# Kernel optimization log

Measured on AMD Instinct MI355X. Metric: run time of the kernel, lower is better.

## Reference

```python
import jax, jax.numpy as jnp
import numpy as np

B, ENC_LEN, DEC_LEN = 4, 1024, 256
ENC_H, DEC_H, ATTN = 1024, 1024, 256


def setup_inputs() -> dict:
    key = jax.random.key(0)
    k1, k2, k3, k4, k5, k6 = jax.random.split(key, 6)
    scale = 0.02
    return {
        "encoded_seq": jax.random.normal(k1, (B, ENC_LEN, ENC_H), jnp.float32),
        "decoder_state": jax.random.normal(k2, (B, DEC_LEN, DEC_H), jnp.float32),
        "input_pad_mask": jnp.ones((B, ENC_LEN), jnp.float32),
        "Wh": jax.random.normal(k3, (ENC_H, ATTN), jnp.float32) * scale,
        "Ws": jax.random.normal(k4, (DEC_H, ATTN), jnp.float32) * scale,
        "bs": jax.random.normal(k5, (ATTN,), jnp.float32) * scale,
        "v": jax.random.normal(k6, (ATTN,), jnp.float32) * scale,
    }


def reference(encoded_seq, decoder_state, input_pad_mask, Wh, Ws, bs, v):
    # projections: [B, dec, A] and [B, enc, A]
    proj_dec = jnp.einsum('bdh,ha->bda', decoder_state, Ws) + bs
    proj_enc = jnp.einsum('beh,ha->bea', encoded_seq, Wh)
    # additive score: tanh(broadcast add) then dot with selector vector v
    added = jnp.tanh(proj_dec[:, :, None, :] + proj_enc[:, None, :, :])  # [B,dec,enc,A]
    attn_logits = jnp.einsum('bdea,a->bde', added, v)                    # [B,dec,enc]
    attn_weights = jax.nn.softmax(attn_logits, axis=-1)
    attn_weights2 = attn_weights * input_pad_mask[:, None, :]
    attn_renorm = attn_weights2 / jnp.sum(attn_weights2, axis=-1, keepdims=True)
    context = jnp.einsum('bde,beh->bdh', attn_renorm, encoded_seq)       # [B,dec,enc_h]
    return context, attn_renorm
```

## Files before the change

### kernel.cpp

```cpp
#include <hip/hip_runtime.h>
#include <hip/hip_bf16.h>

#define BB 4
#define ENC_LEN 1024
#define DEC_LEN 256
#define ENC_H 1024
#define ATTN_A 256

#define C2F 2.8853900817779268f

typedef short bf16x8 __attribute__((ext_vector_type(8)));
typedef float f32x4 __attribute__((ext_vector_type(4)));
typedef unsigned int u32x2 __attribute__((ext_vector_type(2)));

union Q2D {
  uint4 q;
  u32x2 d[2];
};
union BF8 {
  u32x2 d[2];
  bf16x8 v;
};

static __device__ __forceinline__ unsigned short f2bf(float x) {
  union {
    float f;
    unsigned int u;
  } c;
  c.f = x;
  unsigned int r = c.u + 0x7FFFu + ((c.u >> 16) & 1u);
  return (unsigned short)(r >> 16);
}

__global__ __launch_bounds__(256) void prep_k(
    const float* __restrict__ Wh, const float* __restrict__ Ws,
    const float* __restrict__ enc, const float* __restrict__ dec,
    unsigned short* __restrict__ WhT, unsigned short* __restrict__ WsT,
    unsigned short* __restrict__ encT, unsigned short* __restrict__ encB,
    unsigned short* __restrict__ decB) {
  __shared__ unsigned short T[64][68];
  const int wb = blockIdx.x;
  const int t = threadIdx.x;
  const int lr = t >> 4;
  const int lc4 = (t & 15) * 4;

  if (wb >= 1152) {
    const int q = wb - 1152;
    const int r0 = (q >> 4) * 64;
    const int c0 = (q & 15) * 64;
#pragma unroll
    for (int p = 0; p < 4; ++p) {
      const int r = lr + p * 16;
      const float4 v = *(const float4*)&dec[(long)(r0 + r) * ENC_H + c0 + lc4];
      ushort4 o;
      o.x = f2bf(v.x);
      o.y = f2bf(v.y);
      o.z = f2bf(v.z);
      o.w = f2bf(v.w);
      *(ushort4*)&decB[(long)(r0 + r) * ENC_H + c0 + lc4] = o;
    }
    return;
  }

  const float* in;
  unsigned short* out;
  unsigned short* out2 = nullptr;
  int R, C, bx, by;
  if (wb < 128) {
    in = (wb < 64) ? Wh : Ws;
    out = (wb < 64) ? WhT : WsT;
    const int tt = wb & 63;
    R = ENC_H;
    C = ATTN_A;
    bx = tt & 3;
    by = tt >> 2;
  } else {
    const int tt0 = wb - 128;
    const int b = tt0 >> 8;
    const int tt = tt0 & 255;
    in = enc + (long)b * ENC_LEN * ENC_H;
    out = encT + (long)b * ENC_H * ENC_LEN;
    out2 = encB + (long)b * ENC_LEN * ENC_H;
    R = ENC_LEN;
    C = ENC_H;
    bx = tt & 15;
    by = tt >> 4;
  }
  const int r0 = by * 64;
  const int c0 = bx * 64;

#pragma unroll
  for (int p = 0; p < 4; ++p) {
    const int r = lr + p * 16;
    const float4 v = *(const float4*)&in[(long)(r0 + r) * C + c0 + lc4];
    ushort4 o;
    o.x = f2bf(v.x);
    o.y = f2bf(v.y);
    o.z = f2bf(v.z);
    o.w = f2bf(v.w);
    *(ushort4*)&T[r][lc4] = o;
    if (out2) *(ushort4*)&out2[(long)(r0 + r) * C + c0 + lc4] = o;
  }
  __syncthreads();
#pragma unroll
  for (int p = 0; p < 4; ++p) {
    const int c = lr + p * 16;
    ushort4 o;
    o.x = T[lc4 + 0][c];
    o.y = T[lc4 + 1][c];
    o.z = T[lc4 + 2][c];
    o.w = T[lc4 + 3][c];
    *(ushort4*)&out[(long)(c0 + c) * R + r0 + lc4] = o;
  }
}

__global__ __launch_bounds__(256) void pgemm(const unsigned short* __restrict__ decB,
                                             const unsigned short* __restrict__ encB,
                                             const unsigned short* __restrict__ WsT,
                                             const unsigned short* __restrict__ WhT,
                                             float* __restrict__ pdP,
                                             float* __restrict__ peP) {
  __shared__ unsigned short As[64][36];
  __shared__ unsigned short Bs[64][36];
  __shared__ float Cs[64][68];

  const int s = blockIdx.z;
  const bool isPD = blockIdx.y < 16;
  const unsigned short* A = isPD ? decB : encB;
  const unsigned short* BT = isPD ? WsT : WhT;
  const int m0 = (isPD ? blockIdx.y : (blockIdx.y - 16)) * 64;
  const int n0 = blockIdx.x * 64;
  const int kb = s * 512;

  const int tid = threadIdx.x;
  const int lane = tid & 63;
  const int wave = tid >> 6;
  const int quad = lane >> 4;
  const int l16 = lane & 15;
  const int wm = (wave >> 1) * 32;
  const int wn = (wave & 1) * 32;
  const int sr = tid >> 2;
  const int sk = (tid & 3) * 8;

  f32x4 acc[2][2] = {{{0.f, 0.f, 0.f, 0.f}, {0.f, 0.f, 0.f, 0.f}},
                     {{0.f, 0.f, 0.f, 0.f}, {0.f, 0.f, 0.f, 0.f}}};

  const unsigned short* Ap = A + (long)(m0 + sr) * ENC_H + kb + sk;
  const unsigned short* Bp = BT + (long)(n0 + sr) * ENC_H + kb + sk;

  Q2D av, bv;
  av.q = *(const uint4*)(Ap);
  bv.q = *(const uint4*)(Bp);

  for (int k0 = 0; k0 < 512; k0 += 32) {
    __syncthreads();
    *(u32x2*)&As[sr][sk] = av.d[0];
    *(u32x2*)&As[sr][sk + 4] = av.d[1];
    *(u32x2*)&Bs[sr][sk] = bv.d[0];
    *(u32x2*)&Bs[sr][sk + 4] = bv.d[1];
    const int kn = (k0 + 32 < 512) ? (k0 + 32) : 0;
    av.q = *(const uint4*)(Ap + kn);
    bv.q = *(const uint4*)(Bp + kn);
    __syncthreads();

    bf16x8 af[2], bfr[2];
#pragma unroll
    for (int i = 0; i < 2; ++i) {
      BF8 t;
      t.d[0] = *(const u32x2*)&As[wm + i * 16 + l16][quad * 8];
      t.d[1] = *(const u32x2*)&As[wm + i * 16 + l16][quad * 8 + 4];
      af[i] = t.v;
    }
#pragma unroll
    for (int j = 0; j < 2; ++j) {
      BF8 t;
      t.d[0] = *(const u32x2*)&Bs[wn + j * 16 + l16][quad * 8];
      t.d[1] = *(const u32x2*)&Bs[wn + j * 16 + l16][quad * 8 + 4];
      bfr[j] = t.v;
    }
#pragma unroll
    for (int i = 0; i < 2; ++i)
#pragma unroll
      for (int j = 0; j < 2; ++j)
        acc[i][j] = __builtin_amdgcn_mfma_f32_16x16x32_bf16(af[i], bfr[j], acc[i][j],
                                                            0, 0, 0);
  }

  if (isPD) {
    float* out = pdP + (long)s * (1024 * ATTN_A);
#pragma unroll
    for (int j = 0; j < 2; ++j) {
      const int col = n0 + wn + j * 16 + l16;
#pragma unroll
      for (int i = 0; i < 2; ++i) {
        const int row = m0 + wm + i * 16 + quad * 4;
#pragma unroll
        for (int r = 0; r < 4; ++r)
          out[(long)(row + r) * ATTN_A + col] = C2F * acc[i][j][r];
      }
    }
  } else {
    __syncthreads();
#pragma unroll
    for (int i = 0; i < 2; ++i)
#pragma unroll
      for (int j = 0; j < 2; ++j)
#pragma unroll
        for (int r = 0; r < 4; ++r)
          Cs[wn + j * 16 + l16][wm + i * 16 + quad * 4 + r] = C2F * acc[i][j][r];
    __syncthreads();
    const int gb = m0 >> 10;
    const int e0 = m0 & 1023;
    const int et = e0 >> 8;
    const int eoff = e0 & 255;
    float* out = peP + (long)s * (BB * ATTN_A * ENC_LEN) +
                 (long)gb * (ATTN_A * ENC_LEN) + (long)et * (ATTN_A * 256);
#pragma unroll
    for (int p = 0; p < 4; ++p) {
      const int arow = (tid >> 4) + p * 16;
      const int e4 = (tid & 15) * 4;
      const float4 o = *(const float4*)&Cs[arow][e4];
      *(float4*)&out[(long)(n0 + arow) * 256 + eoff + e4] = o;
    }
  }
}

__global__ __launch_bounds__(256) void logits_k(const float* __restrict__ peP,
                                                const float* __restrict__ pdP,
                                                const float* __restrict__ v,
                                                const float* __restrict__ bs,
                                                float* __restrict__ p0,
                                                float* __restrict__ p1,
                                                float* __restrict__ p2,
                                                float* __restrict__ p3) {
  const int tid = threadIdx.x;
  const int et = blockIdx.x;
  const int e = et * 256 + tid;
  const int d0 = blockIdx.y * 8;
  const int b = blockIdx.z >> 2;
  const int aq = blockIdx.z & 3;
  const int a0 = aq * 64;

  __shared__ float EdT[8][64];
  __shared__ float vv[64];

  {
    const int a = tid & 63;
    const int dh = tid >> 6;
    const float cb = C2F * bs[a0 + a];
#pragma unroll
    for (int j = 0; j < 2; ++j) {
      const int dd = dh * 2 + j;
      const long idx = (long)(b * DEC_LEN + d0 + dd) * ATTN_A + a0 + a;
      EdT[dd][a] =
          __builtin_amdgcn_exp2f(pdP[idx] + pdP[idx + 1024 * ATTN_A] + cb);
    }
    if (dh == 0) vv[a] = -2.0f * v[a0 + a];
  }
  __syncthreads();

  float acc[8] = {0.f, 0.f, 0.f, 0.f, 0.f, 0.f, 0.f, 0.f};
  const float* pe0 = peP + (long)b * (ATTN_A * ENC_LEN) + (long)et * (ATTN_A * 256) +
                     (long)a0 * 256 + tid;
  const float* pe1 = pe0 + (long)BB * ATTN_A * ENC_LEN;

  float pA0[4], pA1[4], pB0[4], pB1[4];
#pragma unroll
  for (int u = 0; u < 4; ++u) {
    pA0[u] = pe0[u * 256];
    pA1[u] = pe1[u * 256];
    pB0[u] = pe0[(4 + u) * 256];
    pB1[u] = pe1[(4 + u) * 256];
  }

  for (int a4 = 0; a4 < 64; a4 += 4) {
    float Ee[4];
#pragma unroll
    for (int u = 0; u < 4; ++u) Ee[u] = __builtin_amdgcn_exp2f(pA0[u] + pA1[u]);
    const int an = (a4 + 8 < 64) ? (a4 + 8) : 0;
#pragma unroll
    for (int u = 0; u < 4; ++u) {
      pA0[u] = pB0[u];
      pA1[u] = pB1[u];
      pB0[u] = pe0[(an + u) * 256];
      pB1[u] = pe1[(an + u) * 256];
    }
    const float4 v4 = *(const float4*)&vv[a4];

#pragma unroll
    for (int dd = 0; dd < 8; ++dd) {
      const float4 ed = *(const float4*)&EdT[dd][a4];
      const float dn0 = fmaf(ed.x, Ee[0], 1.0f);
      const float dn1 = fmaf(ed.y, Ee[1], 1.0f);
      const float dn2 = fmaf(ed.z, Ee[2], 1.0f);
      const float dn3 = fmaf(ed.w, Ee[3], 1.0f);
      const float x12 = dn0 * dn1;
      const float x34 = dn2 * dn3;
      float t1 = v4.x * dn1;
      t1 = fmaf(v4.y, dn0, t1);
      float t2 = v4.z * dn3;
      t2 = fmaf(v4.w, dn2, t2);
      float num = t1 * x34;
      num = fmaf(t2, x12, num);
      const float D = x12 * x34;
      const float r = __builtin_amdgcn_rcpf(D);
      acc[dd] = fmaf(num, r, acc[dd]);
    }
  }

  float* po = (aq == 0) ? p0 : (aq == 1) ? p1 : (aq == 2) ? p2 : p3;
  const long base = ((long)(b * DEC_LEN + d0) * ENC_LEN) + e;
#pragma unroll
  for (int dd = 0; dd < 8; ++dd) po[base + (long)dd * ENC_LEN] = acc[dd];
}

__global__ __launch_bounds__(256) void softmax4_k(float* __restrict__ p0,
                                                  const float* __restrict__ p1,
                                                  const float* __restrict__ p2,
                                                  const float* __restrict__ p3,
                                                  const float* __restrict__ mask,
                                                  unsigned short* __restrict__ attnB) {
  const int row = blockIdx.x;
  const int b = row >> 8;
  const int tid = threadIdx.x;
  float* rp = p0 + (long)row * ENC_LEN;
  const float* rq1 = p1 + (long)row * ENC_LEN;
  const float* rq2 = p2 + (long)row * ENC_LEN;
  const float* rq3 = p3 + (long)row * ENC_LEN;
  const float* mp = mask + b * ENC_LEN;
  unsigned short* rb = attnB + (long)row * ENC_LEN;

  float l[4], m[4];
#pragma unroll
  for (int j = 0; j < 4; ++j) {
    const int i = tid + 256 * j;
    l[j] = (rp[i] + rq1[i]) + (rq2[i] + rq3[i]);
    m[j] = mp[i];
  }

  __shared__ float redmax[4];
  __shared__ float redsum[4];
  const int lane = tid & 63;
  const int wid = tid >> 6;

  float tm = fmaxf(fmaxf(l[0], l[1]), fmaxf(l[2], l[3]));
#pragma unroll
  for (int off = 1; off < 64; off <<= 1) tm = fmaxf(tm, __shfl_xor(tm, off, 64));
  if (lane == 0) redmax[wid] = tm;
  __syncthreads();
  const float rmax = fmaxf(fmaxf(redmax[0], redmax[1]), fmaxf(redmax[2], redmax[3]));

  const float LOG2E = 1.4426950408889634f;
  float p[4];
  float ts = 0.f;
#pragma unroll
  for (int j = 0; j < 4; ++j) {
    p[j] = __builtin_amdgcn_exp2f((l[j] - rmax) * LOG2E) * m[j];
    ts += p[j];
  }
#pragma unroll
  for (int off = 1; off < 64; off <<= 1) ts += __shfl_xor(ts, off, 64);
  if (lane == 0) redsum[wid] = ts;
  __syncthreads();
  const float rsum = redsum[0] + redsum[1] + redsum[2] + redsum[3];

  const float inv = 1.0f / rsum;
#pragma unroll
  for (int j = 0; j < 4; ++j) {
    const float w = p[j] * inv;
    rp[tid + 256 * j] = w;
    rb[tid + 256 * j] = f2bf(w);
  }
}

__global__ __launch_bounds__(256) void cgemm(const unsigned short* __restrict__ attnB,
                                             const unsigned short* __restrict__ encT,
                                             float* __restrict__ cP) {
  __shared__ unsigned short As[64][36];
  __shared__ unsigned short Bs[64][36];

  const int b = blockIdx.z >> 1;
  const int s = blockIdx.z & 1;
  const int kb = s * 512;
  const unsigned short* A = attnB + (long)b * DEC_LEN * ENC_LEN;
  const unsigned short* BT = encT + (long)b * ENC_H * ENC_LEN;
  float* C = cP + (long)s * (BB * DEC_LEN * ENC_H) + (long)b * DEC_LEN * ENC_H;

  const int tid = threadIdx.x;
  const int lane = tid & 63;
  const int wave = tid >> 6;
  const int quad = lane >> 4;
  const int l16 = lane & 15;
  const int wm = (wave >> 1) * 32;
  const int wn = (wave & 1) * 32;
  const int m0 = blockIdx.y * 64;
  const int n0 = blockIdx.x * 64;
  const int sr = tid >> 2;
  const int sk = (tid & 3) * 8;

  f32x4 acc[2][2] = {{{0.f, 0.f, 0.f, 0.f}, {0.f, 0.f, 0.f, 0.f}},
                     {{0.f, 0.f, 0.f, 0.f}, {0.f, 0.f, 0.f, 0.f}}};

  const unsigned short* Ap = A + (long)(m0 + sr) * ENC_LEN + kb + sk;
  const unsigned short* Bp = BT + (long)(n0 + sr) * ENC_LEN + kb + sk;

  Q2D av, bv;
  av.q = *(const uint4*)(Ap);
  bv.q = *(const uint4*)(Bp);

  for (int k0 = 0; k0 < 512; k0 += 32) {
    __syncthreads();
    *(u32x2*)&As[sr][sk] = av.d[0];
    *(u32x2*)&As[sr][sk + 4] = av.d[1];
    *(u32x2*)&Bs[sr][sk] = bv.d[0];
    *(u32x2*)&Bs[sr][sk + 4] = bv.d[1];
    const int kn = (k0 + 32 < 512) ? (k0 + 32) : 0;
    av.q = *(const uint4*)(Ap + kn);
    bv.q = *(const uint4*)(Bp + kn);
    __syncthreads();

    bf16x8 af[2], bfr[2];
#pragma unroll
    for (int i = 0; i < 2; ++i) {
      BF8 t;
      t.d[0] = *(const u32x2*)&As[wm + i * 16 + l16][quad * 8];
      t.d[1] = *(const u32x2*)&As[wm + i * 16 + l16][quad * 8 + 4];
      af[i] = t.v;
    }
#pragma unroll
    for (int j = 0; j < 2; ++j) {
      BF8 t;
      t.d[0] = *(const u32x2*)&Bs[wn + j * 16 + l16][quad * 8];
      t.d[1] = *(const u32x2*)&Bs[wn + j * 16 + l16][quad * 8 + 4];
      bfr[j] = t.v;
    }
#pragma unroll
    for (int i = 0; i < 2; ++i)
#pragma unroll
      for (int j = 0; j < 2; ++j)
        acc[i][j] = __builtin_amdgcn_mfma_f32_16x16x32_bf16(af[i], bfr[j], acc[i][j],
                                                            0, 0, 0);
  }

#pragma unroll
  for (int j = 0; j < 2; ++j) {
    const int col = n0 + wn + j * 16 + l16;
#pragma unroll
    for (int i = 0; i < 2; ++i) {
      const int row = m0 + wm + i * 16 + quad * 4;
#pragma unroll
      for (int r = 0; r < 4; ++r) C[(long)(row + r) * ENC_H + col] = acc[i][j][r];
    }
  }
}

__global__ __launch_bounds__(256) void creduce(const float* __restrict__ cP,
                                               float* __restrict__ ctx) {
  const long i = ((long)blockIdx.x * 256 + threadIdx.x) * 4;
  const float4 x = *(const float4*)&cP[i];
  const float4 y = *(const float4*)&cP[i + (long)BB * DEC_LEN * ENC_H];
  float4 o;
  o.x = x.x + y.x;
  o.y = x.y + y.y;
  o.z = x.z + y.z;
  o.w = x.w + y.w;
  *(float4*)&ctx[i] = o;
}

template <int OMODE, bool BIAS>
__global__ __launch_bounds__(256) void gemm64(const float* __restrict__ A,
                                              const float* __restrict__ B,
                                              const float* __restrict__ bias,
                                              float* __restrict__ C,
                                              int K, int lda, int ldb, int ldc,
                                              long sA, long sB, long sC) {
  const int bz = blockIdx.z;
  A += (long)bz * sA;
  B += (long)bz * sB;
  C += (long)bz * sC;

  const int tid = threadIdx.x;
  const int tx = tid & 15;
  const int ty = tid >> 4;

  __shared__ float As2[16][64];
  __shared__ float Bs2[16][64];

  float acc[4][4];
#pragma unroll
  for (int i = 0; i < 4; ++i)
#pragma unroll
    for (int j = 0; j < 4; ++j) acc[i][j] = 0.f;

  const int ar = tid >> 2;
  const int ak4 = (tid & 3) << 2;
  const int br = tid >> 4;
  const int bn4 = (tid & 15) << 2;

  const float* Aload = A + (long)(blockIdx.y * 64 + ar) * lda + ak4;
  const float* Bload = B + (long)br * ldb + blockIdx.x * 64 + bn4;

  for (int k0 = 0; k0 < K; k0 += 16) {
    const float4 av = *(const float4*)(Aload + k0);
    const float4 bv = *(const float4*)(Bload + (long)k0 * ldb);
    __syncthreads();
    As2[ak4 + 0][ar] = av.x;
    As2[ak4 + 1][ar] = av.y;
    As2[ak4 + 2][ar] = av.z;
    As2[ak4 + 3][ar] = av.w;
    *(float4*)&Bs2[br][bn4] = bv;
    __syncthreads();
#pragma unroll
    for (int kk = 0; kk < 16; ++kk) {
      const float4 a4 = *(const float4*)&As2[kk][ty << 2];
      const float4 b4 = *(const float4*)&Bs2[kk][tx << 2];
      const float am[4] = {a4.x, a4.y, a4.z, a4.w};
      const float bn[4] = {b4.x, b4.y, b4.z, b4.w};
#pragma unroll
      for (int i = 0; i < 4; ++i)
#pragma unroll
        for (int j = 0; j < 4; ++j) acc[i][j] = fmaf(am[i], bn[j], acc[i][j]);
    }
  }

  if (OMODE == 0) {
    const int row0 = blockIdx.y * 64 + (ty << 2);
    const int col0 = blockIdx.x * 64 + (tx << 2);
    float4 bb4 = make_float4(0.f, 0.f, 0.f, 0.f);
    if (BIAS) bb4 = *(const float4*)&bias[col0];
#pragma unroll
    for (int i = 0; i < 4; ++i) {
      float4 o;
      o.x = acc[i][0] + bb4.x;
      o.y = acc[i][1] + bb4.y;
      o.z = acc[i][2] + bb4.z;
      o.w = acc[i][3] + bb4.w;
      *(float4*)&C[(long)(row0 + i) * ldc + col0] = o;
    }
  } else {
#pragma unroll
    for (int i = 0; i < 4; ++i) {
      const int gr = blockIdx.y * 64 + (ty << 2) + i;
      const int b = gr >> 10;
      const int e = gr & 1023;
#pragma unroll
      for (int j = 0; j < 4; ++j) {
        const int col = blockIdx.x * 64 + (tx << 2) + j;
        C[(long)b * (ATTN_A * ENC_LEN) + (long)col * ENC_LEN + e] = acc[i][j];
      }
    }
  }
}

__global__ __launch_bounds__(256) void logits_fb(const float* __restrict__ peT,
                                                 const float* __restrict__ pd,
                                                 const float* __restrict__ v,
                                                 float* __restrict__ out) {
  const int tid = threadIdx.x;
  const int e = blockIdx.x * 256 + tid;
  const int d0 = blockIdx.y * 8;
  const int b = blockIdx.z;

  __shared__ float cpd[ATTN_A][8];
  __shared__ float vv[ATTN_A];

  {
    const int a = tid;
#pragma unroll
    for (int dd = 0; dd < 8; ++dd)
      cpd[a][dd] = C2F * pd[((b * DEC_LEN + d0 + dd) * ATTN_A) + a];
    vv[a] = -2.0f * v[a];
  }
  __syncthreads();

  float acc[8] = {0.f, 0.f, 0.f, 0.f, 0.f, 0.f, 0.f, 0.f};
  const float* pe = peT + (long)b * (ATTN_A * ENC_LEN) + e;

  for (int a = 0; a < ATTN_A; a += 4) {
    float pes[4];
#pragma unroll
    for (int u = 0; u < 4; ++u) pes[u] = pe[(long)(a + u) * ENC_LEN];
#pragma unroll
    for (int u = 0; u < 4; ++u) {
      const float cpe = C2F * pes[u];
      const float vu = vv[a + u];
      const float4 c0 = *(const float4*)&cpd[a + u][0];
      const float4 c1 = *(const float4*)&cpd[a + u][4];
      const float cd[8] = {c0.x, c0.y, c0.z, c0.w, c1.x, c1.y, c1.z, c1.w};
#pragma unroll
      for (int dd = 0; dd < 8; ++dd) {
        const float x = cd[dd] + cpe;
        const float ex = __builtin_amdgcn_exp2f(x);
        const float r = __builtin_amdgcn_rcpf(ex + 1.0f);
        acc[dd] = fmaf(vu, r, acc[dd]);
      }
    }
  }

  const long base = ((long)(b * DEC_LEN + d0) * ENC_LEN) + e;
#pragma unroll
  for (int dd = 0; dd < 8; ++dd) out[base + (long)dd * ENC_LEN] = acc[dd];
}

__global__ __launch_bounds__(256) void softmax_fb(float* __restrict__ attn,
                                                  const float* __restrict__ mask) {
  const int row = blockIdx.x;
  const int b = row >> 8;
  const int tid = threadIdx.x;
  float* rp = attn + (long)row * ENC_LEN;
  const float* mp = mask + b * ENC_LEN;

  float l[4], m[4];
#pragma unroll
  for (int j = 0; j < 4; ++j) {
    l[j] = rp[tid + 256 * j];
    m[j] = mp[tid + 256 * j];
  }

  __shared__ float redmax[4];
  __shared__ float redsum[4];
  const int lane = tid & 63;
  const int wid = tid >> 6;

  float tm = fmaxf(fmaxf(l[0], l[1]), fmaxf(l[2], l[3]));
#pragma unroll
  for (int off = 1; off < 64; off <<= 1) tm = fmaxf(tm, __shfl_xor(tm, off, 64));
  if (lane == 0) redmax[wid] = tm;
  __syncthreads();
  const float rmax = fmaxf(fmaxf(redmax[0], redmax[1]), fmaxf(redmax[2], redmax[3]));

  const float LOG2E = 1.4426950408889634f;
  float p[4];
  float ts = 0.f;
#pragma unroll
  for (int j = 0; j < 4; ++j) {
    p[j] = __builtin_amdgcn_exp2f((l[j] - rmax) * LOG2E) * m[j];
    ts += p[j];
  }
#pragma unroll
  for (int off = 1; off < 64; off <<= 1) ts += __shfl_xor(ts, off, 64);
  if (lane == 0) redsum[wid] = ts;
  __syncthreads();
  const float rsum = redsum[0] + redsum[1] + redsum[2] + redsum[3];

  const float inv = 1.0f / rsum;
#pragma unroll
  for (int j = 0; j < 4; ++j) rp[tid + 256 * j] = p[j] * inv;
}

extern "C" void kernel_launch(void* const* d_in, const int* in_sizes, int n_in,
                              void* d_out, int out_size, void* d_ws, size_t ws_size,
                              hipStream_t stream) {
  const float* enc = (const float*)d_in[0];
  const float* dec = (const float*)d_in[1];
  const float* mask = (const float*)d_in[2];
  const float* Wh = (const float*)d_in[3];
  const float* Ws = (const float*)d_in[4];
  const float* bs = (const float*)d_in[5];
  const float* v = (const float*)d_in[6];

  float* ctx = (float*)d_out;
  float* attn = ctx + (long)BB * DEC_LEN * ENC_H;

  const long N_PD = 2L * 1024 * ATTN_A;
  const long N_PE = 2L * BB * ATTN_A * ENC_LEN;
  const long N_P1 = (long)BB * DEC_LEN * ENC_LEN;
  const long N_CP = 2L * BB * DEC_LEN * ENC_H;
  const long N_ENC = (long)BB * ENC_H * ENC_LEN;
  const long N_W = (long)ATTN_A * ENC_H;
  const long N_DEC = 1024L * ENC_H;
  const long N_ATT = (long)BB * DEC_LEN * ENC_LEN;
  const size_t FAST_WS = (N_PD + N_PE + 3 * N_P1 + N_CP) * 4 +
                         (N_ENC + 2 * N_W + N_ENC + N_DEC + N_ATT) * 2;

  if (ws_size >= FAST_WS) {
    float* pdP = (float*)d_ws;
    float* peP = pdP + N_PD;
    float* p1 = peP + N_PE;
    float* p2 = p1 + N_P1;
    float* p3 = p2 + N_P1;
    float* cP = p3 + N_P1;
    unsigned short* encT = (unsigned short*)(cP + N_CP);
    unsigned short* WhT = encT + N_ENC;
    unsigned short* WsT = WhT + N_W;
    unsigned short* encB = WsT + N_W;
    unsigned short* decB = encB + N_ENC;
    unsigned short* attnB = decB + N_DEC;

    prep_k<<<dim3(1408, 1, 1), 256, 0, stream>>>(Wh, Ws, enc, dec, WhT, WsT, encT,
                                                 encB, decB);
    pgemm<<<dim3(4, 80, 2), 256, 0, stream>>>(decB, encB, WsT, WhT, pdP, peP);
    logits_k<<<dim3(4, 32, BB * 4), 256, 0, stream>>>(peP, pdP, v, bs, attn, p1, p2,
                                                      p3);
    softmax4_k<<<dim3(BB * DEC_LEN, 1, 1), 256, 0, stream>>>(attn, p1, p2, p3, mask,
                                                             attnB);
    cgemm<<<dim3(16, 4, BB * 2), 256, 0, stream>>>(attnB, encT, cP);
    creduce<<<dim3(1024, 1, 1), 256, 0, stream>>>(cP, ctx);
  } else {
    float* pd = (float*)d_ws;
    float* peT = pd + (long)BB * DEC_LEN * ATTN_A;

    gemm64<0, true><<<dim3(ATTN_A / 64, (BB * DEC_LEN) / 64, 1), 256, 0, stream>>>(
        dec, Ws, bs, pd, ENC_H, ENC_H, ATTN_A, ATTN_A, 0, 0, 0);
    gemm64<1, false><<<dim3(ATTN_A / 64, (BB * ENC_LEN) / 64, 1), 256, 0, stream>>>(
        enc, Wh, nullptr, peT, ENC_H, ENC_H, ATTN_A, 0, 0, 0, 0);
    logits_fb<<<dim3(ENC_LEN / 256, DEC_LEN / 8, BB), 256, 0, stream>>>(peT, pd, v,
                                                                        attn);
    softmax_fb<<<dim3(BB * DEC_LEN, 1, 1), 256, 0, stream>>>(attn, mask);
    gemm64<0, false><<<dim3(ENC_H / 64, DEC_LEN / 64, BB), 256, 0, stream>>>(
        attn, enc, nullptr, ctx, ENC_LEN, ENC_LEN, ENC_H, ENC_H,
        (long)DEC_LEN * ENC_LEN, (long)ENC_LEN * ENC_H, (long)DEC_LEN * ENC_H);
  }
}
```

Measured before the change: 144.3 us.

## Replace split-K with smaller M tiles in projection and context GEMMs

```diff
diff --git a/kernel.cpp b/kernel.cpp
--- a/kernel.cpp
+++ b/kernel.cpp
@@ -120,56 +120,55 @@
                                              const unsigned short* __restrict__ WhT,
                                              float* __restrict__ pdP,
                                              float* __restrict__ peP) {
-  __shared__ unsigned short As[64][36];
+  __shared__ unsigned short As[32][36];
   __shared__ unsigned short Bs[64][36];
-  __shared__ float Cs[64][68];
-
-  const int s = blockIdx.z;
-  const bool isPD = blockIdx.y < 16;
+  __shared__ float Cs[64][36];
+
+  const bool isPD = blockIdx.y < 32;
   const unsigned short* A = isPD ? decB : encB;
   const unsigned short* BT = isPD ? WsT : WhT;
-  const int m0 = (isPD ? blockIdx.y : (blockIdx.y - 16)) * 64;
+  const int m0 = (isPD ? blockIdx.y : (blockIdx.y - 32)) * 32;
   const int n0 = blockIdx.x * 64;
-  const int kb = s * 512;
 
   const int tid = threadIdx.x;
   const int lane = tid & 63;
   const int wave = tid >> 6;
   const int quad = lane >> 4;
   const int l16 = lane & 15;
-  const int wm = (wave >> 1) * 32;
+  const int wm = (wave >> 1) * 16;
   const int wn = (wave & 1) * 32;
   const int sr = tid >> 2;
+  const int ar = (tid >> 2) & 31;
   const int sk = (tid & 3) * 8;
 
-  f32x4 acc[2][2] = {{{0.f, 0.f, 0.f, 0.f}, {0.f, 0.f, 0.f, 0.f}},
-                     {{0.f, 0.f, 0.f, 0.f}, {0.f, 0.f, 0.f, 0.f}}};
-
-  const unsigned short* Ap = A + (long)(m0 + sr) * ENC_H + kb + sk;
-  const unsigned short* Bp = BT + (long)(n0 + sr) * ENC_H + kb + sk;
+  f32x4 acc[2] = {{0.f, 0.f, 0.f, 0.f}, {0.f, 0.f, 0.f, 0.f}};
+
+  const unsigned short* Ap = A + (long)(m0 + ar) * ENC_H + sk;
+  const unsigned short* Bp = BT + (long)(n0 + sr) * ENC_H + sk;
 
   Q2D av, bv;
-  av.q = *(const uint4*)(Ap);
+  if (tid < 128) av.q = *(const uint4*)(Ap);
   bv.q = *(const uint4*)(Bp);
 
-  for (int k0 = 0; k0 < 512; k0 += 32) {
+  for (int k0 = 0; k0 < 1024; k0 += 32) {
     __syncthreads();
-    *(u32x2*)&As[sr][sk] = av.d[0];
-    *(u32x2*)&As[sr][sk + 4] = av.d[1];
+    if (tid < 128) {
+      *(u32x2*)&As[ar][sk] = av.d[0];
+      *(u32x2*)&As[ar][sk + 4] = av.d[1];
+    }
     *(u32x2*)&Bs[sr][sk] = bv.d[0];
     *(u32x2*)&Bs[sr][sk + 4] = bv.d[1];
-    const int kn = (k0 + 32 < 512) ? (k0 + 32) : 0;
-    av.q = *(const uint4*)(Ap + kn);
+    const int kn = (k0 + 32 < 1024) ? (k0 + 32) : 0;
+    if (tid < 128) av.q = *(const uint4*)(Ap + kn);
     bv.q = *(const uint4*)(Bp + kn);
     __syncthreads();
 
-    bf16x8 af[2], bfr[2];
-#pragma unroll
-    for (int i = 0; i < 2; ++i) {
+    bf16x8 af, bfr[2];
+    {
       BF8 t;
-      t.d[0] = *(const u32x2*)&As[wm + i * 16 + l16][quad * 8];
-      t.d[1] = *(const u32x2*)&As[wm + i * 16 + l16][quad * 8 + 4];
-      af[i] = t.v;
+      t.d[0] = *(const u32x2*)&As[wm + l16][quad * 8];
+      t.d[1] = *(const u32x2*)&As[wm + l16][quad * 8 + 4];
+      af = t.v;
     }
 #pragma unroll
     for (int j = 0; j < 2; ++j) {
@@ -179,46 +178,36 @@
       bfr[j] = t.v;
     }
 #pragma unroll
-    for (int i = 0; i < 2; ++i)
-#pragma unroll
-      for (int j = 0; j < 2; ++j)
-        acc[i][j] = __builtin_amdgcn_mfma_f32_16x16x32_bf16(af[i], bfr[j], acc[i][j],
-                                                            0, 0, 0);
+    for (int j = 0; j < 2; ++j)
+      acc[j] = __builtin_amdgcn_mfma_f32_16x16x32_bf16(af, bfr[j], acc[j], 0, 0, 0);
   }
 
   if (isPD) {
-    float* out = pdP + (long)s * (1024 * ATTN_A);
 #pragma unroll
     for (int j = 0; j < 2; ++j) {
       const int col = n0 + wn + j * 16 + l16;
-#pragma unroll
-      for (int i = 0; i < 2; ++i) {
-        const int row = m0 + wm + i * 16 + quad * 4;
-#pragma unroll
-        for (int r = 0; r < 4; ++r)
-          out[(long)(row + r) * ATTN_A + col] = C2F * acc[i][j][r];
-      }
+      const int row = m0 + wm + quad * 4;
+#pragma unroll
+      for (int r = 0; r < 4; ++r)
+        pdP[(long)(row + r) * ATTN_A + col] = C2F * acc[j][r];
     }
   } else {
-    __syncthreads();
-#pragma unroll
-    for (int i = 0; i < 2; ++i)
-#pragma unroll
-      for (int j = 0; j < 2; ++j)
-#pragma unroll
-        for (int r = 0; r < 4; ++r)
-          Cs[wn + j * 16 + l16][wm + i * 16 + quad * 4 + r] = C2F * acc[i][j][r];
+#pragma unroll
+    for (int j = 0; j < 2; ++j)
+#pragma unroll
+      for (int r = 0; r < 4; ++r)
+        Cs[wn + j * 16 + l16][wm + quad * 4 + r] = C2F * acc[j][r];
     __syncthreads();
     const int gb = m0 >> 10;
     const int e0 = m0 & 1023;
     const int et = e0 >> 8;
     const int eoff = e0 & 255;
-    float* out = peP + (long)s * (BB * ATTN_A * ENC_LEN) +
-                 (long)gb * (ATTN_A * ENC_LEN) + (long)et * (ATTN_A * 256);
-#pragma unroll
-    for (int p = 0; p < 4; ++p) {
-      const int arow = (tid >> 4) + p * 16;
-      const int e4 = (tid & 15) * 4;
+    float* out = peP + (long)gb * (ATTN_A * ENC_LEN) + (long)et * (ATTN_A * 256);
+#pragma unroll
+    for (int p = 0; p < 2; ++p) {
+      const int slot = tid + p * 256;
+      const int arow = slot >> 3;
+      const int e4 = (slot & 7) * 4;
       const float4 o = *(const float4*)&Cs[arow][e4];
       *(float4*)&out[(long)(n0 + arow) * 256 + eoff + e4] = o;
     }
@@ -252,38 +241,32 @@
     for (int j = 0; j < 2; ++j) {
       const int dd = dh * 2 + j;
       const long idx = (long)(b * DEC_LEN + d0 + dd) * ATTN_A + a0 + a;
-      EdT[dd][a] =
-          __builtin_amdgcn_exp2f(pdP[idx] + pdP[idx + 1024 * ATTN_A] + cb);
+      EdT[dd][a] = __builtin_amdgcn_exp2f(pdP[idx] + cb);
     }
     if (dh == 0) vv[a] = -2.0f * v[a0 + a];
   }
   __syncthreads();
 
   float acc[8] = {0.f, 0.f, 0.f, 0.f, 0.f, 0.f, 0.f, 0.f};
-  const float* pe0 = peP + (long)b * (ATTN_A * ENC_LEN) + (long)et * (ATTN_A * 256) +
-                     (long)a0 * 256 + tid;
-  const float* pe1 = pe0 + (long)BB * ATTN_A * ENC_LEN;
-
-  float pA0[4], pA1[4], pB0[4], pB1[4];
+  const float* pe = peP + (long)b * (ATTN_A * ENC_LEN) + (long)et * (ATTN_A * 256) +
+                    (long)a0 * 256 + tid;
+
+  float pA[4], pB[4];
 #pragma unroll
   for (int u = 0; u < 4; ++u) {
-    pA0[u] = pe0[u * 256];
-    pA1[u] = pe1[u * 256];
-    pB0[u] = pe0[(4 + u) * 256];
-    pB1[u] = pe1[(4 + u) * 256];
+    pA[u] = pe[u * 256];
+    pB[u] = pe[(4 + u) * 256];
   }
 
   for (int a4 = 0; a4 < 64; a4 += 4) {
     float Ee[4];
 #pragma unroll
-    for (int u = 0; u < 4; ++u) Ee[u] = __builtin_amdgcn_exp2f(pA0[u] + pA1[u]);
+    for (int u = 0; u < 4; ++u) Ee[u] = __builtin_amdgcn_exp2f(pA[u]);
     const int an = (a4 + 8 < 64) ? (a4 + 8) : 0;
 #pragma unroll
     for (int u = 0; u < 4; ++u) {
-      pA0[u] = pB0[u];
-      pA1[u] = pB1[u];
-      pB0[u] = pe0[(an + u) * 256];
-      pB1[u] = pe1[(an + u) * 256];
+      pA[u] = pB[u];
+      pB[u] = pe[(an + u) * 256];
     }
     const float4 v4 = *(const float4*)&vv[a4];
 
@@ -375,57 +358,56 @@
 
 __global__ __launch_bounds__(256) void cgemm(const unsigned short* __restrict__ attnB,
                                              const unsigned short* __restrict__ encT,
-                                             float* __restrict__ cP) {
-  __shared__ unsigned short As[64][36];
+                                             float* __restrict__ ctx) {
+  __shared__ unsigned short As[32][36];
   __shared__ unsigned short Bs[64][36];
 
-  const int b = blockIdx.z >> 1;
-  const int s = blockIdx.z & 1;
-  const int kb = s * 512;
+  const int b = blockIdx.z;
   const unsigned short* A = attnB + (long)b * DEC_LEN * ENC_LEN;
   const unsigned short* BT = encT + (long)b * ENC_H * ENC_LEN;
-  float* C = cP + (long)s * (BB * DEC_LEN * ENC_H) + (long)b * DEC_LEN * ENC_H;
+  float* C = ctx + (long)b * DEC_LEN * ENC_H;
 
   const int tid = threadIdx.x;
   const int lane = tid & 63;
   const int wave = tid >> 6;
   const int quad = lane >> 4;
   const int l16 = lane & 15;
-  const int wm = (wave >> 1) * 32;
+  const int wm = (wave >> 1) * 16;
   const int wn = (wave & 1) * 32;
-  const int m0 = blockIdx.y * 64;
+  const int m0 = blockIdx.y * 32;
   const int n0 = blockIdx.x * 64;
   const int sr = tid >> 2;
+  const int ar = (tid >> 2) & 31;
   const int sk = (tid & 3) * 8;
 
-  f32x4 acc[2][2] = {{{0.f, 0.f, 0.f, 0.f}, {0.f, 0.f, 0.f, 0.f}},
-                     {{0.f, 0.f, 0.f, 0.f}, {0.f, 0.f, 0.f, 0.f}}};
-
-  const unsigned short* Ap = A + (long)(m0 + sr) * ENC_LEN + kb + sk;
-  const unsigned short* Bp = BT + (long)(n0 + sr) * ENC_LEN + kb + sk;
+  f32x4 acc[2] = {{0.f, 0.f, 0.f, 0.f}, {0.f, 0.f, 0.f, 0.f}};
+
+  const unsigned short* Ap = A + (long)(m0 + ar) * ENC_LEN + sk;
+  const unsigned short* Bp = BT + (long)(n0 + sr) * ENC_LEN + sk;
 
   Q2D av, bv;
-  av.q = *(const uint4*)(Ap);
+  if (tid < 128) av.q = *(const uint4*)(Ap);
   bv.q = *(const uint4*)(Bp);
 
-  for (int k0 = 0; k0 < 512; k0 += 32) {
+  for (int k0 = 0; k0 < 1024; k0 += 32) {
     __syncthreads();
-    *(u32x2*)&As[sr][sk] = av.d[0];
-    *(u32x2*)&As[sr][sk + 4] = av.d[1];
+    if (tid < 128) {
+      *(u32x2*)&As[ar][sk] = av.d[0];
+      *(u32x2*)&As[ar][sk + 4] = av.d[1];
+    }
     *(u32x2*)&Bs[sr][sk] = bv.d[0];
     *(u32x2*)&Bs[sr][sk + 4] = bv.d[1];
-    const int kn = (k0 + 32 < 512) ? (k0 + 32) : 0;
-    av.q = *(const uint4*)(Ap + kn);
+    const int kn = (k0 + 32 < 1024) ? (k0 + 32) : 0;
+    if (tid < 128) av.q = *(const uint4*)(Ap + kn);
     bv.q = *(const uint4*)(Bp + kn);
     __syncthreads();
 
-    bf16x8 af[2], bfr[2];
-#pragma unroll
-    for (int i = 0; i < 2; ++i) {
+    bf16x8 af, bfr[2];
+    {
       BF8 t;
-      t.d[0] = *(const u32x2*)&As[wm + i * 16 + l16][quad * 8];
-      t.d[1] = *(const u32x2*)&As[wm + i * 16 + l16][quad * 8 + 4];
-      af[i] = t.v;
+      t.d[0] = *(const u32x2*)&As[wm + l16][quad * 8];
+      t.d[1] = *(const u32x2*)&As[wm + l16][quad * 8 + 4];
+      af = t.v;
     }
 #pragma unroll
     for (int j = 0; j < 2; ++j) {
@@ -435,36 +417,17 @@
       bfr[j] = t.v;
     }
 #pragma unroll
-    for (int i = 0; i < 2; ++i)
-#pragma unroll
-      for (int j = 0; j < 2; ++j)
-        acc[i][j] = __builtin_amdgcn_mfma_f32_16x16x32_bf16(af[i], bfr[j], acc[i][j],
-                                                            0, 0, 0);
+    for (int j = 0; j < 2; ++j)
+      acc[j] = __builtin_amdgcn_mfma_f32_16x16x32_bf16(af, bfr[j], acc[j], 0, 0, 0);
   }
 
 #pragma unroll
   for (int j = 0; j < 2; ++j) {
     const int col = n0 + wn + j * 16 + l16;
-#pragma unroll
-    for (int i = 0; i < 2; ++i) {
-      const int row = m0 + wm + i * 16 + quad * 4;
-#pragma unroll
-      for (int r = 0; r < 4; ++r) C[(long)(row + r) * ENC_H + col] = acc[i][j][r];
-    }
-  }
-}
-
-__global__ __launch_bounds__(256) void creduce(const float* __restrict__ cP,
-                                               float* __restrict__ ctx) {
-  const long i = ((long)blockIdx.x * 256 + threadIdx.x) * 4;
-  const float4 x = *(const float4*)&cP[i];
-  const float4 y = *(const float4*)&cP[i + (long)BB * DEC_LEN * ENC_H];
-  float4 o;
-  o.x = x.x + y.x;
-  o.y = x.y + y.y;
-  o.z = x.z + y.z;
-  o.w = x.w + y.w;
-  *(float4*)&ctx[i] = o;
+    const int row = m0 + wm + quad * 4;
+#pragma unroll
+    for (int r = 0; r < 4; ++r) C[(long)(row + r) * ENC_H + col] = acc[j][r];
+  }
 }
 
 template <int OMODE, bool BIAS>
@@ -662,15 +625,14 @@
   float* ctx = (float*)d_out;
   float* attn = ctx + (long)BB * DEC_LEN * ENC_H;
 
-  const long N_PD = 2L * 1024 * ATTN_A;
-  const long N_PE = 2L * BB * ATTN_A * ENC_LEN;
+  const long N_PD = 1024L * ATTN_A;
+  const long N_PE = (long)BB * ATTN_A * ENC_LEN;
   const long N_P1 = (long)BB * DEC_LEN * ENC_LEN;
-  const long N_CP = 2L * BB * DEC_LEN * ENC_H;
   const long N_ENC = (long)BB * ENC_H * ENC_LEN;
   const long N_W = (long)ATTN_A * ENC_H;
   const long N_DEC = 1024L * ENC_H;
   const long N_ATT = (long)BB * DEC_LEN * ENC_LEN;
-  const size_t FAST_WS = (N_PD + N_PE + 3 * N_P1 + N_CP) * 4 +
+  const size_t FAST_WS = (N_PD + N_PE + 3 * N_P1) * 4 +
                          (N_ENC + 2 * N_W + N_ENC + N_DEC + N_ATT) * 2;
 
   if (ws_size >= FAST_WS) {
@@ -679,8 +641,7 @@
     float* p1 = peP + N_PE;
     float* p2 = p1 + N_P1;
     float* p3 = p2 + N_P1;
-    float* cP = p3 + N_P1;
-    unsigned short* encT = (unsigned short*)(cP + N_CP);
+    unsigned short* encT = (unsigned short*)(p3 + N_P1);
     unsigned short* WhT = encT + N_ENC;
     unsigned short* WsT = WhT + N_W;
     unsigned short* encB = WsT + N_W;
@@ -689,13 +650,12 @@
 
     prep_k<<<dim3(1408, 1, 1), 256, 0, stream>>>(Wh, Ws, enc, dec, WhT, WsT, encT,
                                                  encB, decB);
-    pgemm<<<dim3(4, 80, 2), 256, 0, stream>>>(decB, encB, WsT, WhT, pdP, peP);
+    pgemm<<<dim3(4, 160, 1), 256, 0, stream>>>(decB, encB, WsT, WhT, pdP, peP);
     logits_k<<<dim3(4, 32, BB * 4), 256, 0, stream>>>(peP, pdP, v, bs, attn, p1, p2,
                                                       p3);
     softmax4_k<<<dim3(BB * DEC_LEN, 1, 1), 256, 0, stream>>>(attn, p1, p2, p3, mask,
                                                              attnB);
-    cgemm<<<dim3(16, 4, BB * 2), 256, 0, stream>>>(attnB, encT, cP);
-    creduce<<<dim3(1024, 1, 1), 256, 0, stream>>>(cP, ctx);
+    cgemm<<<dim3(16, 8, BB), 256, 0, stream>>>(attnB, encT, ctx);
   } else {
     float* pd = (float*)d_ws;
     float* peT = pd + (long)BB * DEC_LEN * ATTN_A;
```

Measured after the change: 144.3 us. About the same (+0.0%).
